# Optimization experiments

Measured on AMD Instinct MI355X. Metric: run time of the kernel, lower is better.

Reference implementation:

```python
import jax, jax.numpy as jnp
import numpy as np

N, M, E, IN, HID = 100000, 2048, 65536, 512, 256
TAU, LAMDA = 0.5, 1.0


def _l2n(a, eps=1e-12):
    # F.normalize: x / max(||x||_2, eps) along dim=1
    return a / jnp.maximum(jnp.linalg.norm(a, axis=1, keepdims=True), eps)


def setup_inputs() -> dict:
    key = jax.random.key(0)
    ks = jax.random.split(key, 16)
    s = 0.05  # weight scale (xavier-like)
    inp = {
        "x": jax.random.normal(ks[0], (N, IN), jnp.float32),
        "We0": jax.random.normal(ks[1], (IN, HID), jnp.float32) * s,
        "be0": jnp.zeros((HID,), jnp.float32),
        "We1": jax.random.normal(ks[2], (HID, HID), jnp.float32) * s,
        "be1": jnp.zeros((HID,), jnp.float32),
        "Wt0": jax.random.normal(ks[3], (IN, HID), jnp.float32) * s,
        "bt0": jnp.zeros((HID,), jnp.float32),
        "Wt1": jax.random.normal(ks[4], (HID, HID), jnp.float32) * s,
        "bt1": jnp.zeros((HID,), jnp.float32),
        "Wp0": jax.random.normal(ks[5], (HID, HID), jnp.float32) * s,
        "bp0": jnp.zeros((HID,), jnp.float32),
        "Wp1": jax.random.normal(ks[6], (HID, HID), jnp.float32) * s,
        "bp1": jnp.zeros((HID,), jnp.float32),
        "p_vals": jnp.ones((N,), jnp.float32),
        "cg_vals": jax.random.uniform(ks[7], (E,), jnp.float32),
        "p_assign": jax.random.randint(ks[8], (N,), 0, M, jnp.int32),
        "cg_rows": jax.random.randint(ks[9], (E,), 0, M, jnp.int32),
        "cg_cols": jax.random.randint(ks[10], (E,), 0, M, jnp.int32),
        "neg_idx": jax.random.randint(ks[11], (N,), 0, M, jnp.int32),
    }
    return inp


def reference(x, We0, be0, We1, be1, Wt0, bt0, Wt1, bt1,
              Wp0, bp0, Wp1, bp1, p_vals, cg_vals,
              p_assign, cg_rows, cg_cols, neg_idx):
    # encoder: stacked Linears, no activation (batch_norm=layer_norm=False)
    h = (x @ We0 + be0) @ We1 + be1                      # [N, HID]
    # h = spmm(P.T, h): per-cluster weighted sum
    hc = jax.ops.segment_sum(p_vals[:, None] * h, p_assign, num_segments=M)  # [M, HID]
    # target encoder
    v = (x @ Wt0 + bt0) @ Wt1 + bt1                      # [N, HID]

    # pos_score: projector (relu between layers, none on last) + normalize
    q = jax.nn.relu(hc @ Wp0 + bp0) @ Wp1 + bp1          # [M, HID]
    q = _l2n(q)
    vn = _l2n(v)
    pos_sim = jnp.sum(vn * q[p_assign], axis=1) / TAU    # [N]
    pos_score = jnp.exp(
        jax.ops.segment_sum(p_vals * pos_sim, p_assign, num_segments=M))[:, None]  # [M,1]

    # neg_score: dense cluster-cluster similarity
    hn = _l2n(hc)
    neg_score = jnp.exp((hn @ hn.T) / TAU)               # [M, M]

    # partition_score = coarse_g @ neg_score (sparse row-scatter)
    partition_score = jax.ops.segment_sum(
        cg_vals[:, None] * neg_score[cg_cols], cg_rows, num_segments=M)  # [M, M]

    loss = jnp.mean(-jnp.log(pos_score + LAMDA * partition_score)
                    + jnp.log(pos_score + neg_score.sum(axis=1)))
    return loss
```

## Files before the change

### kernel.cpp

```cpp
#include <hip/hip_runtime.h>
#include <hip/hip_bf16.h>
#include <math.h>

#define N_PTS  100000
#define M_CL   2048
#define E_EDG  65536
#define IN_DIM 512
#define HID    256

typedef unsigned short u16;
typedef __attribute__((ext_vector_type(8))) short bf16x8;
typedef __attribute__((ext_vector_type(4))) float f32x4;

__device__ __forceinline__ u16 f2bf(float f){
  __hip_bfloat16 h = __float2bfloat16(f);
  return *reinterpret_cast<u16*>(&h);
}
__device__ __forceinline__ unsigned pk2(float a, float b){
  return (unsigned)f2bf(a) | ((unsigned)f2bf(b) << 16);
}
__device__ __forceinline__ float bf2f(u16 v){
  return __uint_as_float((unsigned)v << 16);
}
__device__ __forceinline__ void glds16(const u16* g, u16* l){
  __builtin_amdgcn_global_load_lds(
      (const __attribute__((address_space(1))) unsigned int*)(g),
      (__attribute__((address_space(3))) unsigned int*)(l), 16, 0, 0);
}

static const size_t OFF_POSACC = 0;
static const size_t OFF_NEGSUM = 8192;
static const size_t OFF_HISTP  = 16384;
static const size_t OFF_CURP   = 24576;
static const size_t OFF_HISTE  = 32768;
static const size_t OFF_CURE   = 40960;
static const size_t OFF_LOSS   = 49152;
static const size_t ZERO_BYTES = 49408;
static const size_t OFF_STARTP = 49664;
static const size_t OFF_STARTE = 58112;
static const size_t OFF_SORTPT = 66560;
static const size_t OFF_SCOL   = 466688;
static const size_t OFF_SVAL   = 728832;
static const size_t OFF_CNT    = 990976;
static const size_t OFF_XC     = 999168;
static const size_t OFF_Q      = 9387776;
static const size_t OFF_HNB    = 11484928;
static const size_t OFF_NEGB   = 13582080;
static const size_t OFF_WT0T   = 22020096;
static const size_t OFF_WT1T   = 22282240;
static const size_t OFF_XBF    = 33554432;

__global__ __launch_bounds__(256) void k_zero(unsigned* __restrict__ p, int n){
  int i = blockIdx.x*256 + threadIdx.x;
  if (i < n) p[i] = 0u;
}

__global__ __launch_bounds__(256) void k_hist(const int* __restrict__ idx, int n, int* __restrict__ hist){
  int i = blockIdx.x*256 + threadIdx.x;
  if (i < n) atomicAdd(&hist[idx[i]], 1);
}

__global__ __launch_bounds__(256) void k_scan(const int* __restrict__ hist, int* __restrict__ start){
  __shared__ int part[256];
  int t = threadIdx.x;
  int v[8]; int s = 0;
#pragma unroll
  for (int j=0;j<8;j++){ v[j] = hist[t*8+j]; s += v[j]; }
  part[t] = s;
  __syncthreads();
  if (t == 0){
    int run = 0;
    for (int i=0;i<256;i++){ int tmp = part[i]; part[i] = run; run += tmp; }
  }
  __syncthreads();
  int run = part[t];
#pragma unroll
  for (int j=0;j<8;j++){ start[t*8+j] = run; run += v[j]; }
  if (t == 255) start[M_CL] = run;
}

__global__ __launch_bounds__(256) void k_scatter_pts(const int* __restrict__ assign, const int* __restrict__ start,
                                                     int* __restrict__ cur, int* __restrict__ out){
  int i = blockIdx.x*256 + threadIdx.x;
  if (i < N_PTS){
    int r = assign[i];
    int p = start[r] + atomicAdd(&cur[r], 1);
    out[p] = i;
  }
}

__global__ __launch_bounds__(256) void k_scatter_edges(const int* __restrict__ rows, const int* __restrict__ cols,
                                                       const float* __restrict__ vals, const int* __restrict__ start,
                                                       int* __restrict__ cur, int* __restrict__ scol,
                                                       float* __restrict__ sval){
  int e = blockIdx.x*256 + threadIdx.x;
  if (e < E_EDG){
    int r = rows[e];
    int p = start[r] + atomicAdd(&cur[r], 1);
    scol[p] = cols[e];
    sval[p] = vals[e];
  }
}

__global__ __launch_bounds__(256) void k_cluster_agg(const float* __restrict__ x, const float* __restrict__ pv,
                                                     const int* __restrict__ sorted_pt, const int* __restrict__ start,
                                                     float* __restrict__ Xc, float* __restrict__ cnt,
                                                     u16* __restrict__ xbf){
  const int m = blockIdx.x;
  const int t = threadIdx.x;
  const int half = t >> 7;
  const int u = t & 127;
  const int s0 = start[m], s1 = start[m+1];
  f32x4 a = {0.f,0.f,0.f,0.f};
  float c = 0.f;
  for (int p = s0 + half; p < s1; p += 2){
    int row = sorted_pt[p];
    float w = pv[row];
    f32x4 xv = *reinterpret_cast<const f32x4*>(x + (size_t)row*IN_DIM + u*4);
    a.x = fmaf(w, xv.x, a.x); a.y = fmaf(w, xv.y, a.y);
    a.z = fmaf(w, xv.z, a.z); a.w = fmaf(w, xv.w, a.w);
    c += w;
    uint2 pk; pk.x = pk2(xv.x, xv.y); pk.y = pk2(xv.z, xv.w);
    *reinterpret_cast<uint2*>(xbf + (size_t)row*IN_DIM + u*4) = pk;
  }
  __shared__ __align__(16) float sh[128*4];
  __shared__ float shc[2];
  if (half == 1) *reinterpret_cast<f32x4*>(sh + u*4) = a;
  if (t == 0)   shc[0] = c;
  if (t == 128) shc[1] = c;
  __syncthreads();
  if (half == 0){
    f32x4 b = *reinterpret_cast<const f32x4*>(sh + u*4);
    a.x += b.x; a.y += b.y; a.z += b.z; a.w += b.w;
    *reinterpret_cast<f32x4*>(Xc + (size_t)m*IN_DIM + u*4) = a;
    if (t == 0) cnt[m] = shc[0] + shc[1];
  }
}

template<int K>
__global__ __launch_bounds__(256) void k_transpose_bf16(const float* __restrict__ W, u16* __restrict__ Wt){
  int o = blockIdx.x*256 + threadIdx.x;
  int n = o / K, k = o % K;
  Wt[o] = f2bf(W[(size_t)k*HID + n]);
}

template<int K>
__device__ __forceinline__ void mc_layer(const float* __restrict__ W, const float* act, int t, float acc[4]){
#pragma unroll
  for (int r=0;r<4;r++) acc[r] = 0.f;
#pragma unroll 2
  for (int k=0;k<K;k+=4){
    float w0 = W[(size_t)(k+0)*HID + t];
    float w1 = W[(size_t)(k+1)*HID + t];
    float w2 = W[(size_t)(k+2)*HID + t];
    float w3 = W[(size_t)(k+3)*HID + t];
#pragma unroll
    for (int r=0;r<4;r++){
      float4 av = *reinterpret_cast<const float4*>(act + r*K + k);
      acc[r] = fmaf(av.x, w0, acc[r]);
      acc[r] = fmaf(av.y, w1, acc[r]);
      acc[r] = fmaf(av.z, w2, acc[r]);
      acc[r] = fmaf(av.w, w3, acc[r]);
    }
  }
}

__global__ __launch_bounds__(256) void k_mchain(
    const float* __restrict__ Xc, const float* __restrict__ cnt,
    const float* __restrict__ We0, const float* __restrict__ be0,
    const float* __restrict__ We1, const float* __restrict__ be1,
    const float* __restrict__ Wp0, const float* __restrict__ bp0,
    const float* __restrict__ Wp1, const float* __restrict__ bp1,
    u16* __restrict__ hnb, float* __restrict__ q){
  __shared__ __align__(16) float a_sh[4*512];
  __shared__ __align__(16) float b_sh[4*256];
  __shared__ float part[4][4];
  const int t = threadIdx.x;
  const int rb = blockIdx.x*4;
  for (int i=t; i<4*128; i+=256){
    int r = i>>7, k4 = i&127;
    reinterpret_cast<float4*>(a_sh + r*512)[k4] =
      reinterpret_cast<const float4*>(Xc + (size_t)(rb+r)*IN_DIM)[k4];
  }
  float cv[4];
#pragma unroll
  for (int r=0;r<4;r++) cv[r] = cnt[rb+r];
  __syncthreads();

  float acc[4], v[4];
  mc_layer<512>(We0, a_sh, t, acc);
  {
    float b = be0[t];
#pragma unroll
    for (int r=0;r<4;r++) b_sh[r*256+t] = fmaf(cv[r], b, acc[r]);
  }
  __syncthreads();
  mc_layer<256>(We1, b_sh, t, acc);
  {
    float b = be1[t];
#pragma unroll
    for (int r=0;r<4;r++){
      v[r] = fmaf(cv[r], b, acc[r]);
      float s = v[r]*v[r];
#pragma unroll
      for (int off=32;off;off>>=1) s += __shfl_xor(s, off, 64);
      if ((t&63) == 0) part[t>>6][r] = s;
      a_sh[r*256+t] = v[r];
    }
  }
  __syncthreads();
#pragma unroll
  for (int r=0;r<4;r++){
    float tot = part[0][r]+part[1][r]+part[2][r]+part[3][r];
    float inv = 1.0f / fmaxf(sqrtf(tot), 1e-12f);
    hnb[(size_t)(rb+r)*HID + t] = f2bf(v[r]*inv);
  }
  mc_layer<256>(Wp0, a_sh, t, acc);
  {
    float b = bp0[t];
#pragma unroll
    for (int r=0;r<4;r++) b_sh[r*256+t] = fmaxf(acc[r]+b, 0.f);
  }
  __syncthreads();
  mc_layer<256>(Wp1, b_sh, t, acc);
  {
    float b = bp1[t];
#pragma unroll
    for (int r=0;r<4;r++){
      v[r] = acc[r] + b;
      float s = v[r]*v[r];
#pragma unroll
      for (int off=32;off;off>>=1) s += __shfl_xor(s, off, 64);
      if ((t&63) == 0) part[t>>6][r] = s;
    }
  }
  __syncthreads();
#pragma unroll
  for (int r=0;r<4;r++){
    float tot = part[0][r]+part[1][r]+part[2][r]+part[3][r];
    float inv = 1.0f / fmaxf(sqrtf(tot), 1e-12f);
    q[(size_t)(rb+r)*HID + t] = v[r]*inv;
  }
}

__global__ __launch_bounds__(256,2) void k_target_mfma(
    const u16* __restrict__ xbf, const u16* __restrict__ Wt0t, const float* __restrict__ bt0,
    const u16* __restrict__ Wt1t, const float* __restrict__ bt1,
    const float* __restrict__ q, const int* __restrict__ assign,
    const float* __restrict__ pv, float* __restrict__ posacc){
  __shared__ u16 ws[2*8192];
  __shared__ u16 act[16384];
  __shared__ float red[2][4][4][16];
  u16* xs = act;

  const int t  = threadIdx.x;
  const int w  = t >> 6;
  const int l  = t & 63;
  const int c  = l & 15;
  const int lg = l >> 4;
  const int gm0 = blockIdx.x * 64;

  const int sxr = w*16 + (l>>2);
  int sxg = gm0 + sxr; if (sxg >= N_PTS) sxg = N_PTS-1;
  const u16* xsrc = xbf + (size_t)sxg*IN_DIM + ((l&3) ^ ((sxr>>1)&3))*8;
  u16* xdst = xs + (w*64 + l)*8;

  f32x4 acc[4][4];
#pragma unroll
  for (int i=0;i<4;i++)
#pragma unroll
    for (int j=0;j<4;j++){ acc[i][j].x=0.f; acc[i][j].y=0.f; acc[i][j].z=0.f; acc[i][j].w=0.f; }

  #define STAGE_W(Wt, K, k0, buf) do { \
    _Pragma("unroll") \
    for (int i_=0;i_<4;i_++){ \
      int row_ = w*64 + i_*16 + (l>>2); \
      int ug_  = (l&3) ^ ((row_>>1)&3); \
      glds16((Wt) + (size_t)row_*(K) + (k0) + ug_*8, \
             ws + (buf)*8192 + (w*64 + i_*16)*32 + l*8); \
    } } while(0)
  #define STAGE_X(k0, buf) glds16(xsrc + (k0), xdst + (buf)*2048)

  const int su = lg ^ ((c>>1)&3);

  STAGE_W(Wt0t, IN_DIM, 0, 0);
  STAGE_X(0, 0);
  __syncthreads();
#pragma unroll
  for (int ks=0; ks<16; ks++){
    int buf = ks & 1;
    if (ks < 15){ STAGE_W(Wt0t, IN_DIM, (ks+1)*32, buf^1); STAGE_X((ks+1)*32, buf^1); }
    bf16x8 bfr[4];
#pragma unroll
    for (int mf=0; mf<4; mf++)
      bfr[mf] = *reinterpret_cast<const bf16x8*>(xs + buf*2048 + ((mf*16+c)*4 + su)*8);
#pragma unroll
    for (int nf=0; nf<4; nf++){
      bf16x8 afr = *reinterpret_cast<const bf16x8*>(ws + buf*8192 + ((w*64+nf*16+c)*4 + su)*8);
#pragma unroll
      for (int mf=0; mf<4; mf++)
        acc[mf][nf] = __builtin_amdgcn_mfma_f32_16x16x32_bf16(afr, bfr[mf], acc[mf][nf], 0,0,0);
    }
    __syncthreads();
  }

#pragma unroll
  for (int nf=0; nf<4; nf++){
    f32x4 bias = *reinterpret_cast<const f32x4*>(bt0 + w*64 + nf*16 + lg*4);
#pragma unroll
    for (int mf=0; mf<4; mf++){
      int m = mf*16 + c;
      f32x4 v = acc[mf][nf] + bias;
      uint2 p; p.x = pk2(v.x, v.y); p.y = pk2(v.z, v.w);
      int u = (w*8 + nf*2 + (lg>>1)) ^ (c&7);
      *reinterpret_cast<uint2*>(act + (m*32 + u)*8 + (lg&1)*4) = p;
    }
  }
#pragma unroll
  for (int i=0;i<4;i++)
#pragma unroll
    for (int j=0;j<4;j++){ acc[i][j].x=0.f; acc[i][j].y=0.f; acc[i][j].z=0.f; acc[i][j].w=0.f; }
  STAGE_W(Wt1t, HID, 0, 0);
  __syncthreads();

#pragma unroll
  for (int ks=0; ks<8; ks++){
    int buf = ks & 1;
    if (ks < 7) STAGE_W(Wt1t, HID, (ks+1)*32, buf^1);
    bf16x8 bfr[4];
#pragma unroll
    for (int mf=0; mf<4; mf++){
      int m = mf*16 + c;
      int u = (ks*4 + lg) ^ (c&7);
      bfr[mf] = *reinterpret_cast<const bf16x8*>(act + (m*32 + u)*8);
    }
#pragma unroll
    for (int nf=0; nf<4; nf++){
      bf16x8 afr = *reinterpret_cast<const bf16x8*>(ws + buf*8192 + ((w*64+nf*16+c)*4 + su)*8);
#pragma unroll
      for (int mf=0; mf<4; mf++)
        acc[mf][nf] = __builtin_amdgcn_mfma_f32_16x16x32_bf16(afr, bfr[mf], acc[mf][nf], 0,0,0);
    }
    __syncthreads();
  }

#pragma unroll
  for (int mf=0; mf<4; mf++){
    int gm = gm0 + mf*16 + c;
    int cl = assign[(gm < N_PTS) ? gm : (N_PTS-1)];
    const float* qrow = q + (size_t)cl*HID + w*64 + lg*4;
    float ss = 0.f, d = 0.f;
#pragma unroll
    for (int nf=0; nf<4; nf++){
      f32x4 b  = *reinterpret_cast<const f32x4*>(bt1 + w*64 + nf*16 + lg*4);
      f32x4 qv = *reinterpret_cast<const f32x4*>(qrow + nf*16);
      f32x4 v  = acc[mf][nf] + b;
      ss = fmaf(v.x,v.x, fmaf(v.y,v.y, fmaf(v.z,v.z, fmaf(v.w,v.w, ss))));
      d  = fmaf(v.x,qv.x, fmaf(v.y,qv.y, fmaf(v.z,qv.z, fmaf(v.w,qv.w, d))));
    }
    ss += __shfl_xor(ss, 16, 64); ss += __shfl_xor(ss, 32, 64);
    d  += __shfl_xor(d , 16, 64); d  += __shfl_xor(d , 32, 64);
    if (lg == 0){ red[0][w][mf][c] = ss; red[1][w][mf][c] = d; }
  }
  __syncthreads();
  if (t < 64){
    int gm = gm0 + t;
    if (gm < N_PTS){
      int mf = t>>4, cc = t&15;
      float ss = red[0][0][mf][cc]+red[0][1][mf][cc]+red[0][2][mf][cc]+red[0][3][mf][cc];
      float d  = red[1][0][mf][cc]+red[1][1][mf][cc]+red[1][2][mf][cc]+red[1][3][mf][cc];
      float inv = 1.0f / fmaxf(sqrtf(ss), 1e-12f);
      atomicAdd(&posacc[assign[gm]], pv[gm] * d * inv * 2.0f);
    }
  }
  #undef STAGE_W
  #undef STAGE_X
}

__global__ __launch_bounds__(256,2) void k_neg_mfma(
    const u16* __restrict__ hnb, u16* __restrict__ negb, float* __restrict__ negsum){
  __shared__ u16 wsb[2*8192];
  __shared__ u16 xsb[2*2048];
  const int t  = threadIdx.x;
  const int w  = t >> 6;
  const int l  = t & 63;
  const int c  = l & 15;
  const int lg = l >> 4;
  const int j0 = blockIdx.x * 256;
  const int i0 = blockIdx.y * 64;

  const int sxr = w*16 + (l>>2);
  const u16* xsrc = hnb + (size_t)(i0+sxr)*HID + ((l&3) ^ ((sxr>>1)&3))*8;
  u16* xdst = xsb + (w*64 + l)*8;

  f32x4 acc[4][4];
#pragma unroll
  for (int i=0;i<4;i++)
#pragma unroll
    for (int j=0;j<4;j++){ acc[i][j].x=0.f; acc[i][j].y=0.f; acc[i][j].z=0.f; acc[i][j].w=0.f; }

  #define NSTAGE_W(k0, buf) do { \
    _Pragma("unroll") \
    for (int i_=0;i_<4;i_++){ \
      int row_ = w*64 + i_*16 + (l>>2); \
      int ug_  = (l&3) ^ ((row_>>1)&3); \
      glds16(hnb + (size_t)(j0+row_)*HID + (k0) + ug_*8, \
             wsb + (buf)*8192 + (w*64 + i_*16)*32 + l*8); \
    } } while(0)
  #define NSTAGE_X(k0, buf) glds16(xsrc + (k0), xdst + (buf)*2048)

  NSTAGE_W(0, 0);
  NSTAGE_X(0, 0);
  __syncthreads();
  const int su = lg ^ ((c>>1)&3);
#pragma unroll
  for (int ks=0; ks<8; ks++){
    int buf = ks & 1;
    if (ks < 7){ NSTAGE_W((ks+1)*32, buf^1); NSTAGE_X((ks+1)*32, buf^1); }
    bf16x8 bfr[4];
#pragma unroll
    for (int mf=0; mf<4; mf++)
      bfr[mf] = *reinterpret_cast<const bf16x8*>(xsb + buf*2048 + ((mf*16+c)*4 + su)*8);
#pragma unroll
    for (int nf=0; nf<4; nf++){
      bf16x8 afr = *reinterpret_cast<const bf16x8*>(wsb + buf*8192 + ((w*64+nf*16+c)*4 + su)*8);
#pragma unroll
      for (int mf=0; mf<4; mf++)
        acc[mf][nf] = __builtin_amdgcn_mfma_f32_16x16x32_bf16(afr, bfr[mf], acc[mf][nf], 0,0,0);
    }
    __syncthreads();
  }

#pragma unroll
  for (int mf=0; mf<4; mf++){
    int i = i0 + mf*16 + c;
    float rs = 0.f;
#pragma unroll
    for (int nf=0; nf<4; nf++){
      f32x4 a = acc[mf][nf];
      float e0 = __expf(a.x*2.0f), e1 = __expf(a.y*2.0f);
      float e2 = __expf(a.z*2.0f), e3 = __expf(a.w*2.0f);
      rs += e0+e1+e2+e3;
      uint2 p; p.x = pk2(e0, e1); p.y = pk2(e2, e3);
      *reinterpret_cast<uint2*>(negb + (size_t)i*M_CL + j0 + w*64 + nf*16 + lg*4) = p;
    }
    rs += __shfl_xor(rs, 16, 64); rs += __shfl_xor(rs, 32, 64);
    if (lg == 0) atomicAdd(&negsum[i], rs);
  }
  #undef NSTAGE_W
  #undef NSTAGE_X
}

__global__ __launch_bounds__(256) void k_loss(const u16* __restrict__ negb, const float* __restrict__ negsum,
                                              const float* __restrict__ posacc, const int* __restrict__ start,
                                              const int* __restrict__ scol, const float* __restrict__ sval,
                                              double* __restrict__ loss){
  const int i = blockIdx.x, t = threadIdx.x;
  float ps[8] = {};
  const int s0 = start[i], s1 = start[i+1];
  for (int e=s0;e<s1;e++){
    int c = scol[e];
    float v = sval[e];
    bf16x8 r = *reinterpret_cast<const bf16x8*>(negb + (size_t)c*M_CL + t*8);
#pragma unroll
    for (int jj=0;jj<8;jj++) ps[jj] = fmaf(v, bf2f((u16)r[jj]), ps[jj]);
  }
  float pos = __expf(posacc[i]);
  f32x4 nsa = *reinterpret_cast<const f32x4*>(negsum + t*8);
  f32x4 nsb = *reinterpret_cast<const f32x4*>(negsum + t*8 + 4);
  float ns[8] = {nsa.x,nsa.y,nsa.z,nsa.w,nsb.x,nsb.y,nsb.z,nsb.w};
  float part = 0.f;
#pragma unroll
  for (int jj=0;jj<8;jj++)
    part += __logf(pos + ns[jj]) - __logf(pos + ps[jj]);
#pragma unroll
  for (int off=32;off;off>>=1) part += __shfl_xor(part, off, 64);
  __shared__ float wsum[4];
  if ((t&63) == 0) wsum[t>>6] = part;
  __syncthreads();
  if (t == 0){
    double s = (double)wsum[0] + (double)wsum[1] + (double)wsum[2] + (double)wsum[3];
    atomicAdd(loss, s);
  }
}

__global__ void k_finalize(const double* __restrict__ loss, float* __restrict__ out){
  if (threadIdx.x == 0 && blockIdx.x == 0)
    out[0] = (float)(loss[0] / ((double)M_CL * (double)M_CL));
}

extern "C" void kernel_launch(void* const* d_in, const int* in_sizes, int n_in,
                              void* d_out, int out_size, void* d_ws, size_t ws_size,
                              hipStream_t stream){
  const float* x    = (const float*)d_in[0];
  const float* We0  = (const float*)d_in[1];
  const float* be0  = (const float*)d_in[2];
  const float* We1  = (const float*)d_in[3];
  const float* be1  = (const float*)d_in[4];
  const float* Wt0  = (const float*)d_in[5];
  const float* bt0  = (const float*)d_in[6];
  const float* Wt1  = (const float*)d_in[7];
  const float* bt1  = (const float*)d_in[8];
  const float* Wp0  = (const float*)d_in[9];
  const float* bp0  = (const float*)d_in[10];
  const float* Wp1  = (const float*)d_in[11];
  const float* bp1  = (const float*)d_in[12];
  const float* pv   = (const float*)d_in[13];
  const float* cgv  = (const float*)d_in[14];
  const int*   pas  = (const int*)d_in[15];
  const int*   cgr  = (const int*)d_in[16];
  const int*   cgc  = (const int*)d_in[17];

  char* ws = (char*)d_ws;
  float*  posacc  = (float*)(ws + OFF_POSACC);
  float*  negsum  = (float*)(ws + OFF_NEGSUM);
  int*    hist_p  = (int*)  (ws + OFF_HISTP);
  int*    cur_p   = (int*)  (ws + OFF_CURP);
  int*    hist_e  = (int*)  (ws + OFF_HISTE);
  int*    cur_e   = (int*)  (ws + OFF_CURE);
  double* lossd   = (double*)(ws + OFF_LOSS);
  int*    start_p = (int*)  (ws + OFF_STARTP);
  int*    start_e = (int*)  (ws + OFF_STARTE);
  int*    sortpt  = (int*)  (ws + OFF_SORTPT);
  int*    scol    = (int*)  (ws + OFF_SCOL);
  float*  sval    = (float*)(ws + OFF_SVAL);
  float*  cnt     = (float*)(ws + OFF_CNT);
  float*  Xc      = (float*)(ws + OFF_XC);
  float*  qb      = (float*)(ws + OFF_Q);
  u16*    hnb     = (u16*)  (ws + OFF_HNB);
  u16*    negb    = (u16*)  (ws + OFF_NEGB);
  u16*    Wt0t    = (u16*)  (ws + OFF_WT0T);
  u16*    Wt1t    = (u16*)  (ws + OFF_WT1T);
  u16*    xbf     = (u16*)  (ws + OFF_XBF);

  k_zero<<<(ZERO_BYTES/4 + 255)/256, 256, 0, stream>>>((unsigned*)ws, ZERO_BYTES/4);

  k_hist<<<(N_PTS+255)/256, 256, 0, stream>>>(pas, N_PTS, hist_p);
  k_hist<<<(E_EDG+255)/256, 256, 0, stream>>>(cgr, E_EDG, hist_e);
  k_scan<<<1, 256, 0, stream>>>(hist_p, start_p);
  k_scan<<<1, 256, 0, stream>>>(hist_e, start_e);
  k_scatter_pts<<<(N_PTS+255)/256, 256, 0, stream>>>(pas, start_p, cur_p, sortpt);
  k_scatter_edges<<<(E_EDG+255)/256, 256, 0, stream>>>(cgr, cgc, cgv, start_e, cur_e, scol, sval);

  k_transpose_bf16<IN_DIM><<<IN_DIM, 256, 0, stream>>>(Wt0, Wt0t);
  k_transpose_bf16<HID  ><<<HID,    256, 0, stream>>>(Wt1, Wt1t);

  k_cluster_agg<<<M_CL, 256, 0, stream>>>(x, pv, sortpt, start_p, Xc, cnt, xbf);

  k_mchain<<<M_CL/4, 256, 0, stream>>>(Xc, cnt, We0, be0, We1, be1, Wp0, bp0, Wp1, bp1, hnb, qb);

  k_target_mfma<<<(N_PTS+63)/64, 256, 0, stream>>>(xbf, Wt0t, bt0, Wt1t, bt1, qb, pas, pv, posacc);

  dim3 gneg(M_CL/256, M_CL/64);
  k_neg_mfma<<<gneg, 256, 0, stream>>>(hnb, negb, negsum);

  k_loss<<<M_CL, 256, 0, stream>>>(negb, negsum, posacc, start_e, scol, sval, lossd);
  k_finalize<<<1, 64, 0, stream>>>(lossd, (float*)d_out);
}
```

Baseline: 354.2 us.

## Use per-wave LDS weight tiles and register-loaded X to drop block barriers

In the target-encoder and neg-similarity MFMA kernels, the shared X tile is removed. Each wave now loads its B operand straight from global memory into double-buffered registers and stages only its own 64 weight rows into a private LDS slice. Per-iteration __syncthreads calls are replaced with explicit s_waitcnt vmcnt waits plus sched_barrier, so waves advance independently instead of lock-stepping through block barriers. The cost is that all four waves fetch the same X rows, roughly quadrupling X read traffic (absorbed by cache at best). The neg kernel also drops its min-blocks occupancy hint.

```diff
diff --git a/kernel.cpp b/kernel.cpp
--- a/kernel.cpp
+++ b/kernel.cpp
@@ -22,11 +22,14 @@
 __device__ __forceinline__ float bf2f(u16 v){
   return __uint_as_float((unsigned)v << 16);
 }
-__device__ __forceinline__ void glds16(const u16* g, u16* l){
+__device__ __forceinline__ void glds16(const u16* g, u16* lds_base_uniform){
   __builtin_amdgcn_global_load_lds(
       (const __attribute__((address_space(1))) unsigned int*)(g),
-      (__attribute__((address_space(3))) unsigned int*)(l), 16, 0, 0);
-}
+      (__attribute__((address_space(3))) unsigned int*)(lds_base_uniform), 16, 0, 0);
+}
+#define VMWAIT8() do{ asm volatile("s_waitcnt vmcnt(8)" ::: "memory"); __builtin_amdgcn_sched_barrier(0);}while(0)
+#define VMWAIT4() do{ asm volatile("s_waitcnt vmcnt(4)" ::: "memory"); __builtin_amdgcn_sched_barrier(0);}while(0)
+#define VMWAIT0() do{ asm volatile("s_waitcnt vmcnt(0)" ::: "memory"); __builtin_amdgcn_sched_barrier(0);}while(0)
 
 static const size_t OFF_POSACC = 0;
 static const size_t OFF_NEGSUM = 8192;
@@ -248,10 +251,9 @@
     const u16* __restrict__ Wt1t, const float* __restrict__ bt1,
     const float* __restrict__ q, const int* __restrict__ assign,
     const float* __restrict__ pv, float* __restrict__ posacc){
-  __shared__ u16 ws[2*8192];
+  __shared__ u16 wlds[4][2][2048];
   __shared__ u16 act[16384];
   __shared__ float red[2][4][4][16];
-  u16* xs = act;
 
   const int t  = threadIdx.x;
   const int w  = t >> 6;
@@ -260,48 +262,55 @@
   const int lg = l >> 4;
   const int gm0 = blockIdx.x * 64;
 
-  const int sxr = w*16 + (l>>2);
-  int sxg = gm0 + sxr; if (sxg >= N_PTS) sxg = N_PTS-1;
-  const u16* xsrc = xbf + (size_t)sxg*IN_DIM + ((l&3) ^ ((sxr>>1)&3))*8;
-  u16* xdst = xs + (w*64 + l)*8;
-
-  f32x4 acc[4][4];
-#pragma unroll
-  for (int i=0;i<4;i++)
-#pragma unroll
-    for (int j=0;j<4;j++){ acc[i][j].x=0.f; acc[i][j].y=0.f; acc[i][j].z=0.f; acc[i][j].w=0.f; }
-
-  #define STAGE_W(Wt, K, k0, buf) do { \
+  const int wrow = l >> 2;
+  const int wswz = (l&3) ^ ((wrow>>1)&3);
+
+  #define TSTAGE_W(Wt, K, k0, buf) do { \
     _Pragma("unroll") \
     for (int i_=0;i_<4;i_++){ \
-      int row_ = w*64 + i_*16 + (l>>2); \
-      int ug_  = (l&3) ^ ((row_>>1)&3); \
-      glds16((Wt) + (size_t)row_*(K) + (k0) + ug_*8, \
-             ws + (buf)*8192 + (w*64 + i_*16)*32 + l*8); \
+      int row_ = w*64 + i_*16 + wrow; \
+      glds16((Wt) + (size_t)row_*(K) + (k0) + wswz*8, &wlds[w][buf][i_*512]); \
     } } while(0)
-  #define STAGE_X(k0, buf) glds16(xsrc + (k0), xdst + (buf)*2048)
+
+  const u16* xrow[4];
+#pragma unroll
+  for (int mf=0;mf<4;mf++){
+    int gm = gm0 + mf*16 + c; if (gm > N_PTS-1) gm = N_PTS-1;
+    xrow[mf] = xbf + (size_t)gm*IN_DIM + lg*8;
+  }
+
+  f32x4 acc[4][4];
+#pragma unroll
+  for (int i=0;i<4;i++)
+#pragma unroll
+    for (int j=0;j<4;j++){ acc[i][j].x=0.f; acc[i][j].y=0.f; acc[i][j].z=0.f; acc[i][j].w=0.f; }
 
   const int su = lg ^ ((c>>1)&3);
 
-  STAGE_W(Wt0t, IN_DIM, 0, 0);
-  STAGE_X(0, 0);
-  __syncthreads();
+  bf16x8 xreg[2][4];
+  TSTAGE_W(Wt0t, IN_DIM, 0, 0);
+#pragma unroll
+  for (int mf=0;mf<4;mf++) xreg[0][mf] = *reinterpret_cast<const bf16x8*>(xrow[mf]);
+
 #pragma unroll
   for (int ks=0; ks<16; ks++){
-    int buf = ks & 1;
-    if (ks < 15){ STAGE_W(Wt0t, IN_DIM, (ks+1)*32, buf^1); STAGE_X((ks+1)*32, buf^1); }
-    bf16x8 bfr[4];
-#pragma unroll
-    for (int mf=0; mf<4; mf++)
-      bfr[mf] = *reinterpret_cast<const bf16x8*>(xs + buf*2048 + ((mf*16+c)*4 + su)*8);
+    const int buf = ks & 1;
+    if (ks < 15){
+      TSTAGE_W(Wt0t, IN_DIM, (ks+1)*32, buf^1);
+#pragma unroll
+      for (int mf=0;mf<4;mf++)
+        xreg[buf^1][mf] = *reinterpret_cast<const bf16x8*>(xrow[mf] + (ks+1)*32);
+      VMWAIT8();
+    } else {
+      VMWAIT0();
+    }
 #pragma unroll
     for (int nf=0; nf<4; nf++){
-      bf16x8 afr = *reinterpret_cast<const bf16x8*>(ws + buf*8192 + ((w*64+nf*16+c)*4 + su)*8);
+      bf16x8 afr = *reinterpret_cast<const bf16x8*>(&wlds[w][buf][((nf*16+c)*4 + su)*8]);
 #pragma unroll
       for (int mf=0; mf<4; mf++)
-        acc[mf][nf] = __builtin_amdgcn_mfma_f32_16x16x32_bf16(afr, bfr[mf], acc[mf][nf], 0,0,0);
-    }
-    __syncthreads();
+        acc[mf][nf] = __builtin_amdgcn_mfma_f32_16x16x32_bf16(afr, xreg[buf][mf], acc[mf][nf], 0,0,0);
+    }
   }
 
 #pragma unroll
@@ -320,13 +329,18 @@
   for (int i=0;i<4;i++)
 #pragma unroll
     for (int j=0;j<4;j++){ acc[i][j].x=0.f; acc[i][j].y=0.f; acc[i][j].z=0.f; acc[i][j].w=0.f; }
-  STAGE_W(Wt1t, HID, 0, 0);
-  __syncthreads();
-
+  __syncthreads();
+
+  TSTAGE_W(Wt1t, HID, 0, 0);
 #pragma unroll
   for (int ks=0; ks<8; ks++){
-    int buf = ks & 1;
-    if (ks < 7) STAGE_W(Wt1t, HID, (ks+1)*32, buf^1);
+    const int buf = ks & 1;
+    if (ks < 7){
+      TSTAGE_W(Wt1t, HID, (ks+1)*32, buf^1);
+      VMWAIT4();
+    } else {
+      VMWAIT0();
+    }
     bf16x8 bfr[4];
 #pragma unroll
     for (int mf=0; mf<4; mf++){
@@ -336,12 +350,11 @@
     }
 #pragma unroll
     for (int nf=0; nf<4; nf++){
-      bf16x8 afr = *reinterpret_cast<const bf16x8*>(ws + buf*8192 + ((w*64+nf*16+c)*4 + su)*8);
+      bf16x8 afr = *reinterpret_cast<const bf16x8*>(&wlds[w][buf][((nf*16+c)*4 + su)*8]);
 #pragma unroll
       for (int mf=0; mf<4; mf++)
         acc[mf][nf] = __builtin_amdgcn_mfma_f32_16x16x32_bf16(afr, bfr[mf], acc[mf][nf], 0,0,0);
     }
-    __syncthreads();
   }
 
 #pragma unroll
@@ -373,14 +386,12 @@
       atomicAdd(&posacc[assign[gm]], pv[gm] * d * inv * 2.0f);
     }
   }
-  #undef STAGE_W
-  #undef STAGE_X
-}
-
-__global__ __launch_bounds__(256,2) void k_neg_mfma(
+  #undef TSTAGE_W
+}
+
+__global__ __launch_bounds__(256) void k_neg_mfma(
     const u16* __restrict__ hnb, u16* __restrict__ negb, float* __restrict__ negsum){
-  __shared__ u16 wsb[2*8192];
-  __shared__ u16 xsb[2*2048];
+  __shared__ u16 wlds[4][2][2048];
   const int t  = threadIdx.x;
   const int w  = t >> 6;
   const int l  = t & 63;
@@ -389,46 +400,53 @@
   const int j0 = blockIdx.x * 256;
   const int i0 = blockIdx.y * 64;
 
-  const int sxr = w*16 + (l>>2);
-  const u16* xsrc = hnb + (size_t)(i0+sxr)*HID + ((l&3) ^ ((sxr>>1)&3))*8;
-  u16* xdst = xsb + (w*64 + l)*8;
-
-  f32x4 acc[4][4];
-#pragma unroll
-  for (int i=0;i<4;i++)
-#pragma unroll
-    for (int j=0;j<4;j++){ acc[i][j].x=0.f; acc[i][j].y=0.f; acc[i][j].z=0.f; acc[i][j].w=0.f; }
+  const int wrow = l >> 2;
+  const int wswz = (l&3) ^ ((wrow>>1)&3);
 
   #define NSTAGE_W(k0, buf) do { \
     _Pragma("unroll") \
     for (int i_=0;i_<4;i_++){ \
-      int row_ = w*64 + i_*16 + (l>>2); \
-      int ug_  = (l&3) ^ ((row_>>1)&3); \
-      glds16(hnb + (size_t)(j0+row_)*HID + (k0) + ug_*8, \
-             wsb + (buf)*8192 + (w*64 + i_*16)*32 + l*8); \
+      int row_ = j0 + w*64 + i_*16 + wrow; \
+      glds16(hnb + (size_t)row_*HID + (k0) + wswz*8, &wlds[w][buf][i_*512]); \
     } } while(0)
-  #define NSTAGE_X(k0, buf) glds16(xsrc + (k0), xdst + (buf)*2048)
-
+
+  const u16* irow[4];
+#pragma unroll
+  for (int mf=0;mf<4;mf++)
+    irow[mf] = hnb + (size_t)(i0 + mf*16 + c)*HID + lg*8;
+
+  f32x4 acc[4][4];
+#pragma unroll
+  for (int i=0;i<4;i++)
+#pragma unroll
+    for (int j=0;j<4;j++){ acc[i][j].x=0.f; acc[i][j].y=0.f; acc[i][j].z=0.f; acc[i][j].w=0.f; }
+
+  const int su = lg ^ ((c>>1)&3);
+
+  bf16x8 xreg[2][4];
   NSTAGE_W(0, 0);
-  NSTAGE_X(0, 0);
-  __syncthreads();
-  const int su = lg ^ ((c>>1)&3);
+#pragma unroll
+  for (int mf=0;mf<4;mf++) xreg[0][mf] = *reinterpret_cast<const bf16x8*>(irow[mf]);
+
 #pragma unroll
   for (int ks=0; ks<8; ks++){
-    int buf = ks & 1;
-    if (ks < 7){ NSTAGE_W((ks+1)*32, buf^1); NSTAGE_X((ks+1)*32, buf^1); }
-    bf16x8 bfr[4];
-#pragma unroll
-    for (int mf=0; mf<4; mf++)
-      bfr[mf] = *reinterpret_cast<const bf16x8*>(xsb + buf*2048 + ((mf*16+c)*4 + su)*8);
+    const int buf = ks & 1;
+    if (ks < 7){
+      NSTAGE_W((ks+1)*32, buf^1);
+#pragma unroll
+      for (int mf=0;mf<4;mf++)
+        xreg[buf^1][mf] = *reinterpret_cast<const bf16x8*>(irow[mf] + (ks+1)*32);
+      VMWAIT8();
+    } else {
+      VMWAIT0();
+    }
 #pragma unroll
     for (int nf=0; nf<4; nf++){
-      bf16x8 afr = *reinterpret_cast<const bf16x8*>(wsb + buf*8192 + ((w*64+nf*16+c)*4 + su)*8);
+      bf16x8 afr = *reinterpret_cast<const bf16x8*>(&wlds[w][buf][((nf*16+c)*4 + su)*8]);
 #pragma unroll
       for (int mf=0; mf<4; mf++)
-        acc[mf][nf] = __builtin_amdgcn_mfma_f32_16x16x32_bf16(afr, bfr[mf], acc[mf][nf], 0,0,0);
-    }
-    __syncthreads();
+        acc[mf][nf] = __builtin_amdgcn_mfma_f32_16x16x32_bf16(afr, xreg[buf][mf], acc[mf][nf], 0,0,0);
+    }
   }
 
 #pragma unroll
@@ -448,7 +466,6 @@
     if (lg == 0) atomicAdd(&negsum[i], rs);
   }
   #undef NSTAGE_W
-  #undef NSTAGE_X
 }
 
 __global__ __launch_bounds__(256) void k_loss(const u16* __restrict__ negb, const float* __restrict__ negsum,
```

Result: no change. 360.1 us (+1.7%).
